# Performance work log

Measured on AMD Instinct MI355X. Metric: run time of the kernel, lower is better.

Reference implementation:

```python
import jax, jax.numpy as jnp
import numpy as np

N = 100000      # nodes
E = 1600000     # message-passing edges
P = 1000000     # prediction edges
DIN = 128       # node_in_channels
H = 128         # hidden_channels
DOUT = 64       # out_channels (node embedding)
EIN = 32        # edge_in_channels
EPS = 1e-5


def setup_inputs() -> dict:
    key = jax.random.key(0)
    ks = iter(jax.random.split(key, 48))
    nk = lambda: next(ks)
    rn = lambda shape: jax.random.normal(nk(), shape, dtype=jnp.float32)
    glorot = lambda shape: rn(shape) * (1.0 / np.sqrt(shape[-1]))
    inp = {
        "x": rn((N, DIN)),
        "edge_index": jax.random.randint(nk(), (2, E), 0, N),
        "pred_edge_index": jax.random.randint(nk(), (2, P), 0, N),
        "edge_features": rn((P, EIN)),
        # SAGEConv layer 1: lin_l (aggregated, with bias), lin_r (root, no bias)
        "sage1_Wl": glorot((H, DIN)), "sage1_bl": jnp.zeros((H,), jnp.float32), "sage1_Wr": glorot((H, DIN)),
        "bn1_g": jnp.ones((H,), jnp.float32), "bn1_b": jnp.zeros((H,), jnp.float32),
        "bn1_m": rn((H,)) * 0.1, "bn1_v": jnp.ones((H,), jnp.float32),
        # SAGEConv layer 2
        "sage2_Wl": glorot((DOUT, H)), "sage2_bl": jnp.zeros((DOUT,), jnp.float32), "sage2_Wr": glorot((DOUT, H)),
        # edge MLP: Linear(EIN, H//2) -> BN -> ReLU -> Linear(H//2, H//4)
        "edge_W1": glorot((H // 2, EIN)), "edge_b1": jnp.zeros((H // 2,), jnp.float32),
        "ebn_g": jnp.ones((H // 2,), jnp.float32), "ebn_b": jnp.zeros((H // 2,), jnp.float32),
        "ebn_m": rn((H // 2,)) * 0.1, "ebn_v": jnp.ones((H // 2,), jnp.float32),
        "edge_W2": glorot((H // 4, H // 2)), "edge_b2": jnp.zeros((H // 4,), jnp.float32),
        # predictor: Linear(2*DOUT+H//4, H) -> BN -> ReLU -> Linear(H, H//2) -> BN -> ReLU -> Linear(H//2, 1)
        "p_W1": glorot((H, 2 * DOUT + H // 4)), "p_b1": jnp.zeros((H,), jnp.float32),
        "pbn1_g": jnp.ones((H,), jnp.float32), "pbn1_b": jnp.zeros((H,), jnp.float32),
        "pbn1_m": rn((H,)) * 0.1, "pbn1_v": jnp.ones((H,), jnp.float32),
        "p_W2": glorot((H // 2, H)), "p_b2": jnp.zeros((H // 2,), jnp.float32),
        "pbn2_g": jnp.ones((H // 2,), jnp.float32), "pbn2_b": jnp.zeros((H // 2,), jnp.float32),
        "pbn2_m": rn((H // 2,)) * 0.1, "pbn2_v": jnp.ones((H // 2,), jnp.float32),
        "p_W3": glorot((1, H // 2)), "p_b3": jnp.zeros((1,), jnp.float32),
    }
    return inp


def _bn(h, g, b, m, v):
    # eval-mode BatchNorm1d with running stats
    return (h - m) * (g / jnp.sqrt(v + EPS)) + b


def _sage(h, src, dst, Wl, bl, Wr):
    # PyG SAGEConv (mean aggr): lin_l(mean of h[src] at dst) + lin_r(h)
    msg = jax.ops.segment_sum(h[src], dst, num_segments=N)        # [N, d]
    cnt = jax.ops.segment_sum(jnp.ones((src.shape[0],), h.dtype), dst, num_segments=N)
    agg = msg / jnp.maximum(cnt, 1.0)[:, None]
    return agg @ Wl.T + bl + h @ Wr.T


def reference(x, edge_index, pred_edge_index, edge_features,
              sage1_Wl, sage1_bl, sage1_Wr, bn1_g, bn1_b, bn1_m, bn1_v,
              sage2_Wl, sage2_bl, sage2_Wr,
              edge_W1, edge_b1, ebn_g, ebn_b, ebn_m, ebn_v, edge_W2, edge_b2,
              p_W1, p_b1, pbn1_g, pbn1_b, pbn1_m, pbn1_v,
              p_W2, p_b2, pbn2_g, pbn2_b, pbn2_m, pbn2_v, p_W3, p_b3):
    src, dst = edge_index[0], edge_index[1]
    # GraphSAGE encoder (eval mode: dropout off, BN running stats)
    h = _sage(x, src, dst, sage1_Wl, sage1_bl, sage1_Wr)
    h = jax.nn.relu(_bn(h, bn1_g, bn1_b, bn1_m, bn1_v))
    z = _sage(h, src, dst, sage2_Wl, sage2_bl, sage2_Wr)          # [N, DOUT]
    # edge-pair gather + concat
    combined = jnp.concatenate([z[pred_edge_index[0]], z[pred_edge_index[1]]], axis=-1)  # [P, 2*DOUT]
    # edge feature MLP
    e = edge_features @ edge_W1.T + edge_b1
    e = jax.nn.relu(_bn(e, ebn_g, ebn_b, ebn_m, ebn_v))
    e = e @ edge_W2.T + edge_b2                                   # [P, H//4]
    combined = jnp.concatenate([combined, e], axis=-1)            # [P, 2*DOUT + H//4]
    # predictor MLP
    u = combined @ p_W1.T + p_b1
    u = jax.nn.relu(_bn(u, pbn1_g, pbn1_b, pbn1_m, pbn1_v))
    u = u @ p_W2.T + p_b2
    u = jax.nn.relu(_bn(u, pbn2_g, pbn2_b, pbn2_m, pbn2_v))
    out = u @ p_W3.T + p_b3                                       # [P, 1]
    return out[:, 0]
```

## Files before the change

### kernel.cpp

```cpp
#include <hip/hip_runtime.h>

#define Nn 100000
#define Ee 1600000
#define Pp 1000000
#define EPSf 1e-5f

typedef _Float16 f16x8 __attribute__((ext_vector_type(8)));
typedef _Float16 f16x4 __attribute__((ext_vector_type(4)));
typedef _Float16 f16x2 __attribute__((ext_vector_type(2)));
typedef float f32x4 __attribute__((ext_vector_type(4)));

__device__ __forceinline__ float4 ld4(const float* p) { return *(const float4*)p; }

#define oW1l 0
#define oW1r 16384
#define oW2l 32768
#define oW2r 40960
#define oW1a 49152
#define oW1b 57344
#define oW1c 65536
#define oWe1 69632
#define oWe2 71680
#define oWp2 73728
#define W16_TOTAL 81920

#define BN_TOTAL 608

#define BSH 9
#define NB2 196
#define SCAP2 9216
#define ECHUNK 4096
#define NCHUNK ((Ee + ECHUNK - 1) / ECHUNK)

__global__ __launch_bounds__(256) void prep_kernel(
    const float* __restrict__ x,
    const float* __restrict__ s1Wl, const float* __restrict__ s1Wr,
    const float* __restrict__ s2Wl, const float* __restrict__ s2Wr,
    const float* __restrict__ pW1,  const float* __restrict__ eW1,
    const float* __restrict__ eW2,  const float* __restrict__ pW2,
    const float* __restrict__ eb1,
    const float* __restrict__ ebng, const float* __restrict__ ebnb,
    const float* __restrict__ ebnm, const float* __restrict__ ebnv,
    const float* __restrict__ eb2,
    const float* __restrict__ pb1,
    const float* __restrict__ p1g, const float* __restrict__ p1b,
    const float* __restrict__ p1m, const float* __restrict__ p1v,
    const float* __restrict__ pb2,
    const float* __restrict__ p2g, const float* __restrict__ p2b,
    const float* __restrict__ p2m, const float* __restrict__ p2v,
    const float* __restrict__ pW3,
    _Float16* __restrict__ w16, float* __restrict__ bnA,
    _Float16* __restrict__ x16) {
    int tid = blockIdx.x * 256 + threadIdx.x;
    if (tid < W16_TOTAL) {
        float v;
        if (tid < 16384)      v = s1Wl[tid];
        else if (tid < 32768) v = s1Wr[tid - 16384];
        else if (tid < 40960) v = s2Wl[tid - 32768];
        else if (tid < 49152) v = s2Wr[tid - 40960];
        else if (tid < 57344) { int l = tid - 49152; v = pW1[(l >> 6) * 160 + (l & 63)]; }
        else if (tid < 65536) { int l = tid - 57344; v = pW1[(l >> 6) * 160 + 64 + (l & 63)]; }
        else if (tid < 69632) { int l = tid - 65536; v = pW1[(l >> 5) * 160 + 128 + (l & 31)]; }
        else if (tid < 71680) v = eW1[tid - 69632];
        else if (tid < 73728) v = eW2[tid - 71680];
        else                  v = pW2[tid - 73728];
        w16[tid] = (_Float16)v;
    } else if (tid < W16_TOTAL + BN_TOTAL) {
        int b = tid - W16_TOTAL;
        float v;
        if (b < 64)       v = ebng[b] * rsqrtf(ebnv[b] + EPSf);
        else if (b < 128) { int c = b - 64;  float s = ebng[c] * rsqrtf(ebnv[c] + EPSf);
                            v = (eb1[c] - ebnm[c]) * s + ebnb[c]; }
        else if (b < 256) { int c = b - 128; v = p1g[c] * rsqrtf(p1v[c] + EPSf); }
        else if (b < 384) { int c = b - 256; float s = p1g[c] * rsqrtf(p1v[c] + EPSf);
                            v = (pb1[c] - p1m[c]) * s + p1b[c]; }
        else if (b < 448) { int c = b - 384; v = p2g[c] * rsqrtf(p2v[c] + EPSf); }
        else if (b < 512) { int c = b - 448; float s = p2g[c] * rsqrtf(p2v[c] + EPSf);
                            v = (pb2[c] - p2m[c]) * s + p2b[c]; }
        else if (b < 544) v = eb2[b - 512];
        else              v = pW3[b - 544];
        bnA[b] = v;
    }
    int stride = gridDim.x * 256;
    const int NV = Nn * 128 / 4;
    for (int i = tid; i < NV; i += stride) {
        float4 v = ((const float4*)x)[i];
        f16x4 h = {(_Float16)v.x, (_Float16)v.y, (_Float16)v.z, (_Float16)v.w};
        ((f16x4*)x16)[i] = h;
    }
}

__global__ __launch_bounds__(256) void bucketA_kernel(
    const int* __restrict__ src, const int* __restrict__ dst,
    unsigned* __restrict__ stage, unsigned* __restrict__ gcur) {
    __shared__ unsigned hist[NB2];
    __shared__ unsigned base[NB2];
    const int t = threadIdx.x;
    const int e0 = blockIdx.x * ECHUNK;
    for (int u = t; u < NB2; u += 256) hist[u] = 0u;
    __syncthreads();

    int sv[16], dv[16];
#pragma unroll
    for (int k = 0; k < 16; ++k) {
        int e = e0 + k * 256 + t;
        if (e < Ee) {
            sv[k] = src[e];
            dv[k] = dst[e];
            atomicAdd(&hist[dv[k] >> BSH], 1u);
        } else dv[k] = -1;
    }
    __syncthreads();
    for (int u = t; u < NB2; u += 256) {
        unsigned h = hist[u];
        base[u] = h ? atomicAdd(&gcur[u], h) : 0u;
        hist[u] = 0u;
    }
    __syncthreads();
#pragma unroll
    for (int k = 0; k < 16; ++k) {
        if (dv[k] >= 0) {
            int b = dv[k] >> BSH;
            unsigned p = atomicAdd(&hist[b], 1u);
            stage[(size_t)b * SCAP2 + base[b] + p] =
                ((unsigned)sv[k] << BSH) | (unsigned)(dv[k] & 511);
        }
    }
}

__global__ __launch_bounds__(256) void countC_kernel(
    const unsigned* __restrict__ stage, const unsigned* __restrict__ gcur,
    unsigned* __restrict__ deg) {
    __shared__ unsigned cnt[512];
    const int b = blockIdx.x;
    const int t = threadIdx.x;
    cnt[t] = 0u; cnt[t + 256] = 0u;
    __syncthreads();
    unsigned m = gcur[b];
    const unsigned* sp = stage + (size_t)b * SCAP2;
    for (unsigned i = t; i < m; i += 256)
        atomicAdd(&cnt[sp[i] & 511], 1u);
    __syncthreads();
    int n0 = b << BSH;
    if (n0 + t < Nn)       deg[n0 + t] = cnt[t];
    if (n0 + 256 + t < Nn) deg[n0 + 256 + t] = cnt[t + 256];
}

__global__ __launch_bounds__(1024) void scanA_kernel(const unsigned* __restrict__ deg,
                                                     unsigned* __restrict__ escan,
                                                     unsigned* __restrict__ bsum) {
    __shared__ unsigned s[1024];
    int t = threadIdx.x;
    int gid = blockIdx.x * 1024 + t;
    unsigned v = (gid < Nn) ? deg[gid] : 0u;
    s[t] = v;
    __syncthreads();
    for (int off = 1; off < 1024; off <<= 1) {
        unsigned u = (t >= off) ? s[t - off] : 0u;
        __syncthreads();
        s[t] += u;
        __syncthreads();
    }
    if (gid < Nn) escan[gid] = s[t] - v;
    if (t == 1023) bsum[blockIdx.x] = s[1023];
}

__global__ __launch_bounds__(128) void scanB_kernel(const unsigned* __restrict__ bsum,
                                                    unsigned* __restrict__ boff,
                                                    int nblk) {
    __shared__ unsigned s[128];
    int t = threadIdx.x;
    unsigned v = (t < nblk) ? bsum[t] : 0u;
    s[t] = v;
    __syncthreads();
    for (int off = 1; off < 128; off <<= 1) {
        unsigned u = (t >= off) ? s[t - off] : 0u;
        __syncthreads();
        s[t] += u;
        __syncthreads();
    }
    if (t < nblk) boff[t] = s[t] - v;
}

__global__ __launch_bounds__(1024) void scanC_kernel(const unsigned* __restrict__ escan,
                                                     const unsigned* __restrict__ boff,
                                                     int* __restrict__ rowptr) {
    int t = threadIdx.x;
    int gid = blockIdx.x * 1024 + t;
    if (gid < Nn) rowptr[gid] = (int)(escan[gid] + boff[blockIdx.x]);
    if (gid == 0) rowptr[Nn] = Ee;
}

__global__ __launch_bounds__(256) void scatterE_kernel(
    const unsigned* __restrict__ stage, const unsigned* __restrict__ gcur,
    const int* __restrict__ rowptr, int* __restrict__ elist) {
    __shared__ int lbase[512];
    __shared__ unsigned cur[512];
    const int b = blockIdx.x;
    const int t = threadIdx.x;
    const int n0 = b << BSH;
    lbase[t]       = (n0 + t < Nn)       ? rowptr[n0 + t]       : 0;
    lbase[t + 256] = (n0 + 256 + t < Nn) ? rowptr[n0 + 256 + t] : 0;
    cur[t] = 0u; cur[t + 256] = 0u;
    __syncthreads();
    unsigned m = gcur[b];
    const unsigned* sp = stage + (size_t)b * SCAP2;
    for (unsigned i = t; i < m; i += 256) {
        unsigned v = sp[i];
        int lid = v & 511;
        unsigned p = atomicAdd(&cur[lid], 1u);
        elist[lbase[lid] + p] = (int)(v >> BSH);
    }
}

template<int W>
__global__ __launch_bounds__(256, 8) void aggregate16_kernel(
    const _Float16* __restrict__ feat,
    const int* __restrict__ rowptr,
    const int* __restrict__ elist,
    _Float16* __restrict__ outp) {
    int node = (blockIdx.x * 256 + threadIdx.x) >> 6;
    int lane = threadIdx.x & 63;
    if (node >= Nn) return;
    constexpr int SEGS = W / 8;
    constexpr int RPI  = 64 / SEGS;
    const int r = lane / SEGS, c = lane % SEGS;
    int beg = rowptr[node], end = rowptr[node + 1];
    int n = end - beg;
    float acc[8];
#pragma unroll
    for (int k = 0; k < 8; ++k) acc[k] = 0.f;
    for (int c0 = 0; c0 < n; c0 += 64) {
        int m = min(64, n - c0);
        int se = (lane < m) ? elist[beg + c0 + lane] : 0;
        int iters = (m + RPI - 1) / RPI;
#pragma unroll 4
        for (int i = 0; i < iters; ++i) {
            int j = i * RPI + r;
            int s = __shfl(se, j);
            if (j < m) {
                f16x8 v = *(const f16x8*)(feat + (size_t)s * W + c * 8);
#pragma unroll
                for (int k = 0; k < 8; ++k) acc[k] += (float)v[k];
            }
        }
    }
#pragma unroll
    for (int k = 0; k < 8; ++k) {
#pragma unroll
        for (int off = SEGS; off < 64; off <<= 1)
            acc[k] += __shfl_xor(acc[k], off);
    }
    if (r == 0) {
        float inv = 1.0f / fmaxf((float)n, 1.0f);
        f16x8 o;
#pragma unroll
        for (int k = 0; k < 8; ++k) o[k] = (_Float16)(acc[k] * inv);
        *(f16x8*)(outp + (size_t)node * W + c * 8) = o;
    }
}

__global__ __launch_bounds__(256) void dense1_kernel(
    const _Float16* __restrict__ A1, const _Float16* __restrict__ A2,
    const _Float16* __restrict__ W1, const _Float16* __restrict__ W2,
    const float* __restrict__ lb,
    const float* __restrict__ bng, const float* __restrict__ bnb,
    const float* __restrict__ bnm, const float* __restrict__ bnv,
    _Float16* __restrict__ out) {
    const int t = threadIdx.x;
    const int w = t >> 6, lane = t & 63;
    const int lrow = lane & 15, lq = lane >> 4;
    const int row0 = blockIdx.x * 64 + w * 16;
    const int ld = min(row0 + lrow, Nn - 1);

    f16x8 a1[4], a2[4];
#pragma unroll
    for (int i = 0; i < 4; ++i) {
        a1[i] = *(const f16x8*)(A1 + (size_t)ld * 128 + i * 32 + lq * 8);
        a2[i] = *(const f16x8*)(A2 + (size_t)ld * 128 + i * 32 + lq * 8);
    }
#pragma unroll
    for (int nt = 0; nt < 8; ++nt) {
        const _Float16* w1r = W1 + (size_t)(nt * 16 + lrow) * 128;
        const _Float16* w2r = W2 + (size_t)(nt * 16 + lrow) * 128;
        f32x4 c = {0.f, 0.f, 0.f, 0.f};
#pragma unroll
        for (int i = 0; i < 4; ++i) {
            c = __builtin_amdgcn_mfma_f32_16x16x32_f16(a1[i], *(const f16x8*)(w1r + i * 32 + lq * 8), c, 0, 0, 0);
            c = __builtin_amdgcn_mfma_f32_16x16x32_f16(a2[i], *(const f16x8*)(w2r + i * 32 + lq * 8), c, 0, 0, 0);
        }
        int cc = nt * 16 + lrow;
        float s = bng[cc] * rsqrtf(bnv[cc] + EPSf);
        float h = (lb[cc] - bnm[cc]) * s + bnb[cc];
#pragma unroll
        for (int r = 0; r < 4; ++r) {
            int gr = row0 + lq * 4 + r;
            if (gr < Nn)
                out[(size_t)gr * 128 + cc] = (_Float16)fmaxf(c[r] * s + h, 0.f);
        }
    }
}

__global__ __launch_bounds__(256) void gemmY_kernel(
    const _Float16* __restrict__ A, const _Float16* __restrict__ W,
    _Float16* __restrict__ out) {
    const int t = threadIdx.x;
    const int w = t >> 6, lane = t & 63;
    const int lrow = lane & 15, lq = lane >> 4;
    const int row0 = blockIdx.x * 64 + w * 16;
    const int ld = min(row0 + lrow, Nn - 1);
    f16x8 a[4];
#pragma unroll
    for (int i = 0; i < 4; ++i)
        a[i] = *(const f16x8*)(A + (size_t)ld * 128 + i * 32 + lq * 8);
#pragma unroll
    for (int nt = 0; nt < 4; ++nt) {
        const _Float16* wr = W + (size_t)(nt * 16 + lrow) * 128;
        f32x4 c = {0.f, 0.f, 0.f, 0.f};
#pragma unroll
        for (int i = 0; i < 4; ++i)
            c = __builtin_amdgcn_mfma_f32_16x16x32_f16(a[i], *(const f16x8*)(wr + i * 32 + lq * 8), c, 0, 0, 0);
        int cc = nt * 16 + lrow;
#pragma unroll
        for (int r = 0; r < 4; ++r) {
            int gr = row0 + lq * 4 + r;
            if (gr < Nn) out[(size_t)gr * 64 + cc] = (_Float16)c[r];
        }
    }
}

__global__ __launch_bounds__(256) void dense2b_kernel(
    const _Float16* __restrict__ aggY, const _Float16* __restrict__ A2,
    const _Float16* __restrict__ W2, const float* __restrict__ lb,
    _Float16* __restrict__ out) {
    const int t = threadIdx.x;
    const int w = t >> 6, lane = t & 63;
    const int lrow = lane & 15, lq = lane >> 4;
    const int row0 = blockIdx.x * 64 + w * 16;
    const int ld = min(row0 + lrow, Nn - 1);
    f16x8 a[4];
#pragma unroll
    for (int i = 0; i < 4; ++i)
        a[i] = *(const f16x8*)(A2 + (size_t)ld * 128 + i * 32 + lq * 8);
#pragma unroll
    for (int nt = 0; nt < 4; ++nt) {
        const _Float16* wr = W2 + (size_t)(nt * 16 + lrow) * 128;
        f32x4 c = {0.f, 0.f, 0.f, 0.f};
#pragma unroll
        for (int i = 0; i < 4; ++i)
            c = __builtin_amdgcn_mfma_f32_16x16x32_f16(a[i], *(const f16x8*)(wr + i * 32 + lq * 8), c, 0, 0, 0);
        int cc = nt * 16 + lrow;
        float b = lb[cc];
#pragma unroll
        for (int r = 0; r < 4; ++r) {
            int gr = row0 + lq * 4 + r;
            if (gr < Nn) {
                float g = (float)aggY[(size_t)gr * 64 + cc];
                out[(size_t)gr * 64 + cc] = (_Float16)(c[r] + g + b);
            }
        }
    }
}

__global__ __launch_bounds__(256) void emlp_kernel(
    const float* __restrict__ ef,
    const _Float16* __restrict__ w16,
    const float* __restrict__ bnA,
    _Float16* __restrict__ e2out) {
    __shared__ __align__(16) _Float16 E1[64 * 72];
    const int t = threadIdx.x;
    const int lane = t & 63, w = t >> 6;
    const int lrow = lane & 15, lq = lane >> 4;
    const int e0 = blockIdx.x * 64 + w * 16;
    const int erow = w * 16 + lrow;

    const float* src = ef + (size_t)(e0 + lrow) * 32 + lq * 8;
    float4 f0 = ld4(src), f1 = ld4(src + 4);
    f16x8 bf = {(_Float16)f0.x, (_Float16)f0.y, (_Float16)f0.z, (_Float16)f0.w,
                (_Float16)f1.x, (_Float16)f1.y, (_Float16)f1.z, (_Float16)f1.w};

#pragma unroll
    for (int nt = 0; nt < 4; ++nt) {
        f16x8 wf = *(const f16x8*)(w16 + oWe1 + (nt * 16 + lrow) * 32 + lq * 8);
        f32x4 c = {0.f, 0.f, 0.f, 0.f};
        c = __builtin_amdgcn_mfma_f32_16x16x32_f16(wf, bf, c, 0, 0, 0);
        int cb = nt * 16 + lq * 4;
        float4 s = *(const float4*)(bnA + cb);
        float4 h = *(const float4*)(bnA + 64 + cb);
        f16x4 o;
        o[0] = (_Float16)fmaxf(c[0] * s.x + h.x, 0.f);
        o[1] = (_Float16)fmaxf(c[1] * s.y + h.y, 0.f);
        o[2] = (_Float16)fmaxf(c[2] * s.z + h.z, 0.f);
        o[3] = (_Float16)fmaxf(c[3] * s.w + h.w, 0.f);
        *(f16x4*)(E1 + erow * 72 + cb) = o;
    }
    f16x8 a0 = *(const f16x8*)(E1 + erow * 72 + lq * 8);
    f16x8 a1 = *(const f16x8*)(E1 + erow * 72 + 32 + lq * 8);
#pragma unroll
    for (int nt = 0; nt < 2; ++nt) {
        f16x8 b0 = *(const f16x8*)(w16 + oWe2 + (nt * 16 + lrow) * 64 + lq * 8);
        f16x8 b1 = *(const f16x8*)(w16 + oWe2 + (nt * 16 + lrow) * 64 + 32 + lq * 8);
        f32x4 c = {0.f, 0.f, 0.f, 0.f};
        c = __builtin_amdgcn_mfma_f32_16x16x32_f16(b0, a0, c, 0, 0, 0);
        c = __builtin_amdgcn_mfma_f32_16x16x32_f16(b1, a1, c, 0, 0, 0);
        int cb = nt * 16 + lq * 4;
        float4 bias = *(const float4*)(bnA + 512 + cb);
        f16x4 o;
        o[0] = (_Float16)(c[0] + bias.x);
        o[1] = (_Float16)(c[1] + bias.y);
        o[2] = (_Float16)(c[2] + bias.z);
        o[3] = (_Float16)(c[3] + bias.w);
        *(f16x4*)(e2out + (size_t)(e0 + lrow) * 32 + cb) = o;
    }
}

#define EPB 256
#define NT  ((Pp + EPB - 1) / EPB)
#define EGRID 256

#define oL_W1a 0
#define oL_W1b 18432
#define oL_W1c 36864
#define oL_Wp2 47104
#define oL_BN  64512
#define oL_ZU  66304
#define SMEM_BYTES 135936

__global__ __launch_bounds__(1024, 4) void edge_kernel(
    const int* __restrict__ pe,
    const _Float16* __restrict__ e2,
    const _Float16* __restrict__ z,
    const _Float16* __restrict__ w16,
    const float* __restrict__ bnA,
    const float* __restrict__ pb3,
    float* __restrict__ out) {
    __shared__ __align__(16) unsigned char smem[SMEM_BYTES];
    _Float16* LW1a = (_Float16*)(smem + oL_W1a);
    _Float16* LW1b = (_Float16*)(smem + oL_W1b);
    _Float16* LW1c = (_Float16*)(smem + oL_W1c);
    _Float16* LWp2 = (_Float16*)(smem + oL_Wp2);
    float*    LBN  = (float*)(smem + oL_BN);
    _Float16* ZU   = (_Float16*)(smem + oL_ZU);

    const float* bn2s = LBN;        const float* bn2h = LBN + 128;
    const float* bn3s = LBN + 256;  const float* bn3h = LBN + 320;
    const float* wp3g = LBN + 384;

    const int t = threadIdx.x;
    const int lane = t & 63;
    const int w = t >> 6;
    const int m0 = w * 16;
    const int lrow = lane & 15;
    const int lq = lane >> 4;
    const float pb3v = pb3[0];

    auto load_idx = [&](int tl, int& ia, int& ib) {
        int e = min(tl * EPB + m0 + lrow, Pp - 1);
        ia = pe[e];
        ib = pe[Pp + e];
    };
    auto gather = [&](int tl, int ia, int ib, f16x8* F) {
        F[0] = *(const f16x8*)(z + (size_t)ia * 64 + lq * 8);
        F[1] = *(const f16x8*)(z + (size_t)ia * 64 + 32 + lq * 8);
        F[2] = *(const f16x8*)(z + (size_t)ib * 64 + lq * 8);
        F[3] = *(const f16x8*)(z + (size_t)ib * 64 + 32 + lq * 8);
        int e = min(tl * EPB + m0 + lrow, Pp - 1);
        F[4] = *(const f16x8*)(e2 + (size_t)e * 32 + lq * 8);
    };

    int tile = blockIdx.x;
    int ia1, ib1;
    {
        int ia0, ib0;
        load_idx(tile, ia0, ib0);
        load_idx(tile + EGRID, ia1, ib1);
        f16x8 F[5];
        gather(tile, ia0, ib0, F);

        { int r = t >> 3, s = t & 7;
          *(f16x8*)(LW1a + r * 72 + s * 8) = *(const f16x8*)(w16 + oW1a + r * 64 + s * 8);
          *(f16x8*)(LW1b + r * 72 + s * 8) = *(const f16x8*)(w16 + oW1b + r * 64 + s * 8); }
        if (t < 512) { int r = t >> 2, s = t & 3;
          *(f16x8*)(LW1c + r * 40 + s * 8) = *(const f16x8*)(w16 + oW1c + r * 32 + s * 8); }
        { int r = t >> 4, s = t & 15;
          *(f16x8*)(LWp2 + r * 136 + s * 8) = *(const f16x8*)(w16 + oWp2 + r * 128 + s * 8); }
        if (t < 384) LBN[t] = bnA[128 + t];
        else if (t < 448) LBN[t] = bnA[544 + (t - 384)];
        __syncthreads();

        const int erow = m0 + lrow;
        const int zr = erow * 136;
        for (; tile < NT; tile += EGRID) {
            f16x8 G[5];
            gather(tile + EGRID, ia1, ib1, G);
            int ia2, ib2;
            load_idx(tile + 2 * EGRID, ia2, ib2);

            const bool act = (tile * EPB + m0) < Pp;
            if (act) {
                __builtin_amdgcn_s_setprio(1);
#pragma unroll
                for (int nt = 0; nt < 8; ++nt) {
                    const _Float16* wa = LW1a + (nt * 16 + lrow) * 72;
                    const _Float16* wb = LW1b + (nt * 16 + lrow) * 72;
                    const _Float16* wc = LW1c + (nt * 16 + lrow) * 40;
                    f32x4 c = {0.f, 0.f, 0.f, 0.f};
                    c = __builtin_amdgcn_mfma_f32_16x16x32_f16(*(const f16x8*)(wa + lq * 8),      F[0], c, 0, 0, 0);
                    c = __builtin_amdgcn_mfma_f32_16x16x32_f16(*(const f16x8*)(wa + 32 + lq * 8), F[1], c, 0, 0, 0);
                    c = __builtin_amdgcn_mfma_f32_16x16x32_f16(*(const f16x8*)(wb + lq * 8),      F[2], c, 0, 0, 0);
                    c = __builtin_amdgcn_mfma_f32_16x16x32_f16(*(const f16x8*)(wb + 32 + lq * 8), F[3], c, 0, 0, 0);
                    c = __builtin_amdgcn_mfma_f32_16x16x32_f16(*(const f16x8*)(wc + lq * 8),      F[4], c, 0, 0, 0);
                    int cb = nt * 16 + lq * 4;
                    float4 s = *(const float4*)(bn2s + cb);
                    float4 h = *(const float4*)(bn2h + cb);
                    f16x4 o;
                    o[0] = (_Float16)fmaxf(c[0] * s.x + h.x, 0.f);
                    o[1] = (_Float16)fmaxf(c[1] * s.y + h.y, 0.f);
                    o[2] = (_Float16)fmaxf(c[2] * s.z + h.z, 0.f);
                    o[3] = (_Float16)fmaxf(c[3] * s.w + h.w, 0.f);
                    *(f16x4*)(ZU + zr + cb) = o;
                }
                __builtin_amdgcn_s_setprio(0);
                {
                    f16x8 a0 = *(const f16x8*)(ZU + zr + 0  + lq * 8);
                    f16x8 a1 = *(const f16x8*)(ZU + zr + 32 + lq * 8);
                    f16x8 a2 = *(const f16x8*)(ZU + zr + 64 + lq * 8);
                    f16x8 a3 = *(const f16x8*)(ZU + zr + 96 + lq * 8);
                    float acc = 0.f;
                    __builtin_amdgcn_s_setprio(1);
#pragma unroll
                    for (int nt = 0; nt < 4; ++nt) {
                        const _Float16* wr = LWp2 + (nt * 16 + lrow) * 136 + lq * 8;
                        f32x4 c = {0.f, 0.f, 0.f, 0.f};
                        c = __builtin_amdgcn_mfma_f32_16x16x32_f16(*(const f16x8*)(wr + 0),  a0, c, 0, 0, 0);
                        c = __builtin_amdgcn_mfma_f32_16x16x32_f16(*(const f16x8*)(wr + 32), a1, c, 0, 0, 0);
                        c = __builtin_amdgcn_mfma_f32_16x16x32_f16(*(const f16x8*)(wr + 64), a2, c, 0, 0, 0);
                        c = __builtin_amdgcn_mfma_f32_16x16x32_f16(*(const f16x8*)(wr + 96), a3, c, 0, 0, 0);
                        int cb = nt * 16 + lq * 4;
                        float4 s  = *(const float4*)(bn3s + cb);
                        float4 h  = *(const float4*)(bn3h + cb);
                        float4 w3 = *(const float4*)(wp3g + cb);
                        acc += fmaxf(c[0] * s.x + h.x, 0.f) * w3.x;
                        acc += fmaxf(c[1] * s.y + h.y, 0.f) * w3.y;
                        acc += fmaxf(c[2] * s.z + h.z, 0.f) * w3.z;
                        acc += fmaxf(c[3] * s.w + h.w, 0.f) * w3.w;
                    }
                    __builtin_amdgcn_s_setprio(0);
                    acc += __shfl_xor(acc, 16);
                    acc += __shfl_xor(acc, 32);
                    if (lane < 16) out[tile * EPB + m0 + lane] = acc + pb3v;
                }
            }
#pragma unroll
            for (int i = 0; i < 5; ++i) F[i] = G[i];
            ia1 = ia2; ib1 = ib2;
        }
    }
}

extern "C" void kernel_launch(void* const* d_in, const int* in_sizes, int n_in,
                              void* d_out, int out_size, void* d_ws, size_t ws_size,
                              hipStream_t stream) {
    const float* x    = (const float*)d_in[0];
    const int*   eidx = (const int*)d_in[1];
    const int*   pe   = (const int*)d_in[2];
    const float* ef   = (const float*)d_in[3];
    const float* s1Wl = (const float*)d_in[4];
    const float* s1bl = (const float*)d_in[5];
    const float* s1Wr = (const float*)d_in[6];
    const float* bn1g = (const float*)d_in[7];
    const float* bn1b = (const float*)d_in[8];
    const float* bn1m = (const float*)d_in[9];
    const float* bn1v = (const float*)d_in[10];
    const float* s2Wl = (const float*)d_in[11];
    const float* s2bl = (const float*)d_in[12];
    const float* s2Wr = (const float*)d_in[13];
    const float* eW1  = (const float*)d_in[14];
    const float* eb1  = (const float*)d_in[15];
    const float* ebng = (const float*)d_in[16];
    const float* ebnb = (const float*)d_in[17];
    const float* ebnm = (const float*)d_in[18];
    const float* ebnv = (const float*)d_in[19];
    const float* eW2  = (const float*)d_in[20];
    const float* eb2  = (const float*)d_in[21];
    const float* pW1  = (const float*)d_in[22];
    const float* pb1  = (const float*)d_in[23];
    const float* p1g  = (const float*)d_in[24];
    const float* p1b  = (const float*)d_in[25];
    const float* p1m  = (const float*)d_in[26];
    const float* p1v  = (const float*)d_in[27];
    const float* pW2  = (const float*)d_in[28];
    const float* pb2  = (const float*)d_in[29];
    const float* p2g  = (const float*)d_in[30];
    const float* p2b  = (const float*)d_in[31];
    const float* p2m  = (const float*)d_in[32];
    const float* p2v  = (const float*)d_in[33];
    const float* pW3  = (const float*)d_in[34];
    const float* pb3  = (const float*)d_in[35];
    float* out = (float*)d_out;

    char* wk = (char*)d_ws;
    auto carve = [&](size_t bytes) {
        char* p = wk;
        wk += (bytes + 255) & ~(size_t)255;
        return p;
    };
    unsigned*  deg    = (unsigned*)carve((size_t)Nn * 4);
    unsigned*  gcur   = (unsigned*)carve((size_t)256 * 4);
    int*       rowptr = (int*)carve((size_t)(Nn + 1) * 4);
    int*       elist  = (int*)carve((size_t)Ee * 4);
    unsigned*  escan  = (unsigned*)carve((size_t)Nn * 4);
    unsigned*  bsum   = (unsigned*)carve(128 * 4);
    unsigned*  boff   = (unsigned*)carve(128 * 4);
    _Float16*  w16    = (_Float16*)carve((size_t)W16_TOTAL * 2);
    float*     bnA    = (float*)carve((size_t)BN_TOTAL * 4);
    _Float16*  bufX   = (_Float16*)carve((size_t)Nn * 128 * 2);
    _Float16*  bufA   = (_Float16*)carve((size_t)Nn * 128 * 2);
    _Float16*  bufH   = (_Float16*)carve((size_t)Nn * 128 * 2);
    _Float16*  e2buf  = (_Float16*)carve((size_t)Pp * 32 * 2);
    _Float16*  bufY   = bufX;
    _Float16*  bufZ   = bufX + (size_t)Nn * 64;
    _Float16*  bufAy  = bufA;
    unsigned*  stage  = (unsigned*)bufH;

    const int* e_src = eidx;
    const int* e_dst = eidx + Ee;
    const int SBLK = (Nn + 1023) / 1024;

    hipMemsetAsync(gcur, 0, 256 * 4, stream);

    prep_kernel<<<800, 256, 0, stream>>>(x, s1Wl, s1Wr, s2Wl, s2Wr, pW1, eW1, eW2, pW2,
                                         eb1, ebng, ebnb, ebnm, ebnv, eb2,
                                         pb1, p1g, p1b, p1m, p1v,
                                         pb2, p2g, p2b, p2m, p2v, pW3,
                                         w16, bnA, bufX);
    emlp_kernel<<<Pp / 64, 256, 0, stream>>>(ef, w16, bnA, e2buf);

    bucketA_kernel<<<NCHUNK, 256, 0, stream>>>(e_src, e_dst, stage, gcur);
    countC_kernel<<<NB2, 256, 0, stream>>>(stage, gcur, deg);
    scanA_kernel<<<SBLK, 1024, 0, stream>>>(deg, escan, bsum);
    scanB_kernel<<<1, 128, 0, stream>>>(bsum, boff, SBLK);
    scanC_kernel<<<SBLK, 1024, 0, stream>>>(escan, boff, rowptr);
    scatterE_kernel<<<NB2, 256, 0, stream>>>(stage, gcur, rowptr, elist);

    aggregate16_kernel<128><<<Nn / 4, 256, 0, stream>>>(bufX, rowptr, elist, bufA);
    dense1_kernel<<<(Nn + 63) / 64, 256, 0, stream>>>(
        bufA, bufX, w16 + oW1l, w16 + oW1r, s1bl, bn1g, bn1b, bn1m, bn1v, bufH);

    gemmY_kernel<<<(Nn + 63) / 64, 256, 0, stream>>>(bufH, w16 + oW2l, bufY);
    aggregate16_kernel<64><<<Nn / 4, 256, 0, stream>>>(bufY, rowptr, elist, bufAy);
    dense2b_kernel<<<(Nn + 63) / 64, 256, 0, stream>>>(
        bufAy, bufH, w16 + oW2r, s2bl, bufZ);

    edge_kernel<<<EGRID, 1024, 0, stream>>>(pe, e2buf, bufZ, w16, bnA, pb3, out);
}
```

Before: 670.6 us.

## Merge preprocessing kernels, collapse CSR scans, and fuse dense1 with layer-2 GEMM

Prep, edge-feature MLP and edge bucketing now run as one heterogeneous launch, with blocks dispatched by index range. The emlp branch reads fp32 weights and BN parameters directly instead of waiting for prep output. The count, three-stage scan and scatter sequence becomes a single 196-entry bucket scan plus a scatter kernel that builds local prefix sums and writes rowptr itself. dense1 keeps the hidden tile in shared memory and computes the layer-2 Y projection in the same kernel, which removes the gemmY launch and a full re-read of H. Output stores are vectorised by swapping MFMA operand order. The cost is more register and shared-memory pressure in the merged kernels and redundant weight conversion in every emlp block.

```diff
diff --git a/kernel.cpp b/kernel.cpp
--- a/kernel.cpp
+++ b/kernel.cpp
@@ -7,7 +7,6 @@
 
 typedef _Float16 f16x8 __attribute__((ext_vector_type(8)));
 typedef _Float16 f16x4 __attribute__((ext_vector_type(4)));
-typedef _Float16 f16x2 __attribute__((ext_vector_type(2)));
 typedef float f32x4 __attribute__((ext_vector_type(4)));
 
 __device__ __forceinline__ float4 ld4(const float* p) { return *(const float4*)p; }
@@ -32,7 +31,11 @@
 #define ECHUNK 4096
 #define NCHUNK ((Ee + ECHUNK - 1) / ECHUNK)
 
-__global__ __launch_bounds__(256) void prep_kernel(
+#define EMLP_B (Pp / 64)
+#define PREP_B 800
+#define PH1_GRID (NCHUNK + EMLP_B + PREP_B)
+
+__global__ __launch_bounds__(256) void phase1_kernel(
     const float* __restrict__ x,
     const float* __restrict__ s1Wl, const float* __restrict__ s1Wr,
     const float* __restrict__ s2Wl, const float* __restrict__ s2Wr,
@@ -50,161 +53,193 @@
     const float* __restrict__ p2m, const float* __restrict__ p2v,
     const float* __restrict__ pW3,
     _Float16* __restrict__ w16, float* __restrict__ bnA,
-    _Float16* __restrict__ x16) {
-    int tid = blockIdx.x * 256 + threadIdx.x;
-    if (tid < W16_TOTAL) {
-        float v;
-        if (tid < 16384)      v = s1Wl[tid];
-        else if (tid < 32768) v = s1Wr[tid - 16384];
-        else if (tid < 40960) v = s2Wl[tid - 32768];
-        else if (tid < 49152) v = s2Wr[tid - 40960];
-        else if (tid < 57344) { int l = tid - 49152; v = pW1[(l >> 6) * 160 + (l & 63)]; }
-        else if (tid < 65536) { int l = tid - 57344; v = pW1[(l >> 6) * 160 + 64 + (l & 63)]; }
-        else if (tid < 69632) { int l = tid - 65536; v = pW1[(l >> 5) * 160 + 128 + (l & 31)]; }
-        else if (tid < 71680) v = eW1[tid - 69632];
-        else if (tid < 73728) v = eW2[tid - 71680];
-        else                  v = pW2[tid - 73728];
-        w16[tid] = (_Float16)v;
-    } else if (tid < W16_TOTAL + BN_TOTAL) {
-        int b = tid - W16_TOTAL;
-        float v;
-        if (b < 64)       v = ebng[b] * rsqrtf(ebnv[b] + EPSf);
-        else if (b < 128) { int c = b - 64;  float s = ebng[c] * rsqrtf(ebnv[c] + EPSf);
-                            v = (eb1[c] - ebnm[c]) * s + ebnb[c]; }
-        else if (b < 256) { int c = b - 128; v = p1g[c] * rsqrtf(p1v[c] + EPSf); }
-        else if (b < 384) { int c = b - 256; float s = p1g[c] * rsqrtf(p1v[c] + EPSf);
-                            v = (pb1[c] - p1m[c]) * s + p1b[c]; }
-        else if (b < 448) { int c = b - 384; v = p2g[c] * rsqrtf(p2v[c] + EPSf); }
-        else if (b < 512) { int c = b - 448; float s = p2g[c] * rsqrtf(p2v[c] + EPSf);
-                            v = (pb2[c] - p2m[c]) * s + p2b[c]; }
-        else if (b < 544) v = eb2[b - 512];
-        else              v = pW3[b - 544];
-        bnA[b] = v;
-    }
-    int stride = gridDim.x * 256;
-    const int NV = Nn * 128 / 4;
-    for (int i = tid; i < NV; i += stride) {
-        float4 v = ((const float4*)x)[i];
-        f16x4 h = {(_Float16)v.x, (_Float16)v.y, (_Float16)v.z, (_Float16)v.w};
-        ((f16x4*)x16)[i] = h;
-    }
-}
-
-__global__ __launch_bounds__(256) void bucketA_kernel(
-    const int* __restrict__ src, const int* __restrict__ dst,
-    unsigned* __restrict__ stage, unsigned* __restrict__ gcur) {
-    __shared__ unsigned hist[NB2];
-    __shared__ unsigned base[NB2];
+    _Float16* __restrict__ x16,
+    const int* __restrict__ esrc, const int* __restrict__ edst,
+    unsigned* __restrict__ stage, unsigned* __restrict__ gcur,
+    const float* __restrict__ ef, _Float16* __restrict__ e2out) {
+    __shared__ __align__(16) unsigned char sm[9216];
+    const int bb = blockIdx.x;
     const int t = threadIdx.x;
-    const int e0 = blockIdx.x * ECHUNK;
-    for (int u = t; u < NB2; u += 256) hist[u] = 0u;
+
+    if (bb < NCHUNK) {
+        unsigned* hist = (unsigned*)sm;
+        unsigned* base = hist + NB2;
+        const int e0 = bb * ECHUNK;
+        for (int u = t; u < NB2; u += 256) hist[u] = 0u;
+        __syncthreads();
+        int sv[16], dv[16];
+#pragma unroll
+        for (int k = 0; k < 16; ++k) {
+            int e = e0 + k * 256 + t;
+            if (e < Ee) {
+                sv[k] = esrc[e];
+                dv[k] = edst[e];
+                atomicAdd(&hist[dv[k] >> BSH], 1u);
+            } else dv[k] = -1;
+        }
+        __syncthreads();
+        for (int u = t; u < NB2; u += 256) {
+            unsigned h = hist[u];
+            base[u] = h ? atomicAdd(&gcur[u], h) : 0u;
+            hist[u] = 0u;
+        }
+        __syncthreads();
+#pragma unroll
+        for (int k = 0; k < 16; ++k) {
+            if (dv[k] >= 0) {
+                int b = dv[k] >> BSH;
+                unsigned p = atomicAdd(&hist[b], 1u);
+                stage[(size_t)b * SCAP2 + base[b] + p] =
+                    ((unsigned)sv[k] << BSH) | (unsigned)(dv[k] & 511);
+            }
+        }
+    } else if (bb < NCHUNK + EMLP_B) {
+        _Float16* E1 = (_Float16*)sm;
+        const int lane = t & 63, w = t >> 6;
+        const int lrow = lane & 15, lq = lane >> 4;
+        const int e0 = (bb - NCHUNK) * 64 + w * 16;
+        const int erow = w * 16 + lrow;
+
+        const float* src = ef + (size_t)(e0 + lrow) * 32 + lq * 8;
+        float4 f0 = ld4(src), f1 = ld4(src + 4);
+        f16x8 bf = {(_Float16)f0.x, (_Float16)f0.y, (_Float16)f0.z, (_Float16)f0.w,
+                    (_Float16)f1.x, (_Float16)f1.y, (_Float16)f1.z, (_Float16)f1.w};
+#pragma unroll
+        for (int nt = 0; nt < 4; ++nt) {
+            const float* wp = eW1 + (nt * 16 + lrow) * 32 + lq * 8;
+            float4 w0 = ld4(wp), w1 = ld4(wp + 4);
+            f16x8 wf = {(_Float16)w0.x, (_Float16)w0.y, (_Float16)w0.z, (_Float16)w0.w,
+                        (_Float16)w1.x, (_Float16)w1.y, (_Float16)w1.z, (_Float16)w1.w};
+            f32x4 c = {0.f, 0.f, 0.f, 0.f};
+            c = __builtin_amdgcn_mfma_f32_16x16x32_f16(wf, bf, c, 0, 0, 0);
+            int cb = nt * 16 + lq * 4;
+            float4 g = ld4(ebng + cb), vv = ld4(ebnv + cb);
+            float4 b_ = ld4(ebnb + cb), mm = ld4(ebnm + cb), b1 = ld4(eb1 + cb);
+            float sx = g.x * rsqrtf(vv.x + EPSf), hx = (b1.x - mm.x) * sx + b_.x;
+            float sy = g.y * rsqrtf(vv.y + EPSf), hy = (b1.y - mm.y) * sy + b_.y;
+            float sz = g.z * rsqrtf(vv.z + EPSf), hz = (b1.z - mm.z) * sz + b_.z;
+            float sw = g.w * rsqrtf(vv.w + EPSf), hw = (b1.w - mm.w) * sw + b_.w;
+            f16x4 o;
+            o[0] = (_Float16)fmaxf(c[0] * sx + hx, 0.f);
+            o[1] = (_Float16)fmaxf(c[1] * sy + hy, 0.f);
+            o[2] = (_Float16)fmaxf(c[2] * sz + hz, 0.f);
+            o[3] = (_Float16)fmaxf(c[3] * sw + hw, 0.f);
+            *(f16x4*)(E1 + erow * 72 + cb) = o;
+        }
+        f16x8 a0 = *(const f16x8*)(E1 + erow * 72 + lq * 8);
+        f16x8 a1 = *(const f16x8*)(E1 + erow * 72 + 32 + lq * 8);
+#pragma unroll
+        for (int nt = 0; nt < 2; ++nt) {
+            const float* wp = eW2 + (nt * 16 + lrow) * 64 + lq * 8;
+            float4 p0 = ld4(wp), p1 = ld4(wp + 4);
+            float4 q0 = ld4(wp + 32), q1 = ld4(wp + 36);
+            f16x8 b0 = {(_Float16)p0.x, (_Float16)p0.y, (_Float16)p0.z, (_Float16)p0.w,
+                        (_Float16)p1.x, (_Float16)p1.y, (_Float16)p1.z, (_Float16)p1.w};
+            f16x8 b1 = {(_Float16)q0.x, (_Float16)q0.y, (_Float16)q0.z, (_Float16)q0.w,
+                        (_Float16)q1.x, (_Float16)q1.y, (_Float16)q1.z, (_Float16)q1.w};
+            f32x4 c = {0.f, 0.f, 0.f, 0.f};
+            c = __builtin_amdgcn_mfma_f32_16x16x32_f16(b0, a0, c, 0, 0, 0);
+            c = __builtin_amdgcn_mfma_f32_16x16x32_f16(b1, a1, c, 0, 0, 0);
+            int cb = nt * 16 + lq * 4;
+            float4 bias = ld4(eb2 + cb);
+            f16x4 o;
+            o[0] = (_Float16)(c[0] + bias.x);
+            o[1] = (_Float16)(c[1] + bias.y);
+            o[2] = (_Float16)(c[2] + bias.z);
+            o[3] = (_Float16)(c[3] + bias.w);
+            *(f16x4*)(e2out + (size_t)(e0 + lrow) * 32 + cb) = o;
+        }
+    } else {
+        int tid = (bb - NCHUNK - EMLP_B) * 256 + t;
+        if (tid < W16_TOTAL) {
+            float v;
+            if (tid < 16384)      v = s1Wl[tid];
+            else if (tid < 32768) v = s1Wr[tid - 16384];
+            else if (tid < 40960) v = s2Wl[tid - 32768];
+            else if (tid < 49152) v = s2Wr[tid - 40960];
+            else if (tid < 57344) { int l = tid - 49152; v = pW1[(l >> 6) * 160 + (l & 63)]; }
+            else if (tid < 65536) { int l = tid - 57344; v = pW1[(l >> 6) * 160 + 64 + (l & 63)]; }
+            else if (tid < 69632) { int l = tid - 65536; v = pW1[(l >> 5) * 160 + 128 + (l & 31)]; }
+            else if (tid < 71680) v = eW1[tid - 69632];
+            else if (tid < 73728) v = eW2[tid - 71680];
+            else                  v = pW2[tid - 73728];
+            w16[tid] = (_Float16)v;
+        } else if (tid < W16_TOTAL + BN_TOTAL) {
+            int b = tid - W16_TOTAL;
+            float v;
+            if (b < 64)       v = ebng[b] * rsqrtf(ebnv[b] + EPSf);
+            else if (b < 128) { int c = b - 64;  float s = ebng[c] * rsqrtf(ebnv[c] + EPSf);
+                                v = (eb1[c] - ebnm[c]) * s + ebnb[c]; }
+            else if (b < 256) { int c = b - 128; v = p1g[c] * rsqrtf(p1v[c] + EPSf); }
+            else if (b < 384) { int c = b - 256; float s = p1g[c] * rsqrtf(p1v[c] + EPSf);
+                                v = (pb1[c] - p1m[c]) * s + p1b[c]; }
+            else if (b < 448) { int c = b - 384; v = p2g[c] * rsqrtf(p2v[c] + EPSf); }
+            else if (b < 512) { int c = b - 448; float s = p2g[c] * rsqrtf(p2v[c] + EPSf);
+                                v = (pb2[c] - p2m[c]) * s + p2b[c]; }
+            else if (b < 544) v = eb2[b - 512];
+            else              v = pW3[b - 544];
+            bnA[b] = v;
+        }
+        const int NV = Nn * 128 / 4;
+        for (int i = tid; i < NV; i += PREP_B * 256) {
+            float4 v = ((const float4*)x)[i];
+            f16x4 h = {(_Float16)v.x, (_Float16)v.y, (_Float16)v.z, (_Float16)v.w};
+            ((f16x4*)x16)[i] = h;
+        }
+    }
+}
+
+__global__ __launch_bounds__(256) void scanG_kernel(const unsigned* __restrict__ gcur,
+                                                    unsigned* __restrict__ gbase,
+                                                    int* __restrict__ rowptr) {
+    __shared__ unsigned s[256];
+    int t = threadIdx.x;
+    unsigned v = (t < NB2) ? gcur[t] : 0u;
+    s[t] = v;
     __syncthreads();
-
-    int sv[16], dv[16];
-#pragma unroll
-    for (int k = 0; k < 16; ++k) {
-        int e = e0 + k * 256 + t;
-        if (e < Ee) {
-            sv[k] = src[e];
-            dv[k] = dst[e];
-            atomicAdd(&hist[dv[k] >> BSH], 1u);
-        } else dv[k] = -1;
-    }
-    __syncthreads();
-    for (int u = t; u < NB2; u += 256) {
-        unsigned h = hist[u];
-        base[u] = h ? atomicAdd(&gcur[u], h) : 0u;
-        hist[u] = 0u;
-    }
-    __syncthreads();
-#pragma unroll
-    for (int k = 0; k < 16; ++k) {
-        if (dv[k] >= 0) {
-            int b = dv[k] >> BSH;
-            unsigned p = atomicAdd(&hist[b], 1u);
-            stage[(size_t)b * SCAP2 + base[b] + p] =
-                ((unsigned)sv[k] << BSH) | (unsigned)(dv[k] & 511);
-        }
-    }
-}
-
-__global__ __launch_bounds__(256) void countC_kernel(
+    for (int off = 1; off < 256; off <<= 1) {
+        unsigned u = (t >= off) ? s[t - off] : 0u;
+        __syncthreads();
+        s[t] += u;
+        __syncthreads();
+    }
+    if (t < NB2) gbase[t] = s[t] - v;
+    if (t == 0) rowptr[Nn] = Ee;
+}
+
+__global__ __launch_bounds__(256) void scatterE2_kernel(
     const unsigned* __restrict__ stage, const unsigned* __restrict__ gcur,
-    unsigned* __restrict__ deg) {
+    const unsigned* __restrict__ gbase,
+    int* __restrict__ rowptr, int* __restrict__ elist) {
     __shared__ unsigned cnt[512];
+    __shared__ unsigned cur[512];
+    __shared__ int lbase[512];
     const int b = blockIdx.x;
     const int t = threadIdx.x;
+    const int n0 = b << BSH;
     cnt[t] = 0u; cnt[t + 256] = 0u;
     __syncthreads();
-    unsigned m = gcur[b];
+    const unsigned m = gcur[b];
     const unsigned* sp = stage + (size_t)b * SCAP2;
     for (unsigned i = t; i < m; i += 256)
         atomicAdd(&cnt[sp[i] & 511], 1u);
     __syncthreads();
-    int n0 = b << BSH;
-    if (n0 + t < Nn)       deg[n0 + t] = cnt[t];
-    if (n0 + 256 + t < Nn) deg[n0 + 256 + t] = cnt[t + 256];
-}
-
-__global__ __launch_bounds__(1024) void scanA_kernel(const unsigned* __restrict__ deg,
-                                                     unsigned* __restrict__ escan,
-                                                     unsigned* __restrict__ bsum) {
-    __shared__ unsigned s[1024];
-    int t = threadIdx.x;
-    int gid = blockIdx.x * 1024 + t;
-    unsigned v = (gid < Nn) ? deg[gid] : 0u;
-    s[t] = v;
+    unsigned o0 = cnt[t], o1 = cnt[t + 256];
+    for (int off = 1; off < 512; off <<= 1) {
+        unsigned a0 = (t >= off) ? cnt[t - off] : 0u;
+        unsigned a1 = ((t + 256) >= off) ? cnt[t + 256 - off] : 0u;
+        __syncthreads();
+        cnt[t] += a0; cnt[t + 256] += a1;
+        __syncthreads();
+    }
+    const unsigned gb = gbase[b];
+    int r0 = (int)(gb + cnt[t] - o0);
+    int r1 = (int)(gb + cnt[t + 256] - o1);
+    lbase[t] = r0; lbase[t + 256] = r1;
+    cur[t] = 0u; cur[t + 256] = 0u;
+    if (n0 + t < Nn)       rowptr[n0 + t] = r0;
+    if (n0 + 256 + t < Nn) rowptr[n0 + 256 + t] = r1;
     __syncthreads();
-    for (int off = 1; off < 1024; off <<= 1) {
-        unsigned u = (t >= off) ? s[t - off] : 0u;
-        __syncthreads();
-        s[t] += u;
-        __syncthreads();
-    }
-    if (gid < Nn) escan[gid] = s[t] - v;
-    if (t == 1023) bsum[blockIdx.x] = s[1023];
-}
-
-__global__ __launch_bounds__(128) void scanB_kernel(const unsigned* __restrict__ bsum,
-                                                    unsigned* __restrict__ boff,
-                                                    int nblk) {
-    __shared__ unsigned s[128];
-    int t = threadIdx.x;
-    unsigned v = (t < nblk) ? bsum[t] : 0u;
-    s[t] = v;
-    __syncthreads();
-    for (int off = 1; off < 128; off <<= 1) {
-        unsigned u = (t >= off) ? s[t - off] : 0u;
-        __syncthreads();
-        s[t] += u;
-        __syncthreads();
-    }
-    if (t < nblk) boff[t] = s[t] - v;
-}
-
-__global__ __launch_bounds__(1024) void scanC_kernel(const unsigned* __restrict__ escan,
-                                                     const unsigned* __restrict__ boff,
-                                                     int* __restrict__ rowptr) {
-    int t = threadIdx.x;
-    int gid = blockIdx.x * 1024 + t;
-    if (gid < Nn) rowptr[gid] = (int)(escan[gid] + boff[blockIdx.x]);
-    if (gid == 0) rowptr[Nn] = Ee;
-}
-
-__global__ __launch_bounds__(256) void scatterE_kernel(
-    const unsigned* __restrict__ stage, const unsigned* __restrict__ gcur,
-    const int* __restrict__ rowptr, int* __restrict__ elist) {
-    __shared__ int lbase[512];
-    __shared__ unsigned cur[512];
-    const int b = blockIdx.x;
-    const int t = threadIdx.x;
-    const int n0 = b << BSH;
-    lbase[t]       = (n0 + t < Nn)       ? rowptr[n0 + t]       : 0;
-    lbase[t + 256] = (n0 + 256 + t < Nn) ? rowptr[n0 + 256 + t] : 0;
-    cur[t] = 0u; cur[t + 256] = 0u;
-    __syncthreads();
-    unsigned m = gcur[b];
-    const unsigned* sp = stage + (size_t)b * SCAP2;
     for (unsigned i = t; i < m; i += 256) {
         unsigned v = sp[i];
         int lid = v & 511;
@@ -260,18 +295,21 @@
     }
 }
 
-__global__ __launch_bounds__(256) void dense1_kernel(
+__global__ __launch_bounds__(256) void dense1g_kernel(
     const _Float16* __restrict__ A1, const _Float16* __restrict__ A2,
     const _Float16* __restrict__ W1, const _Float16* __restrict__ W2,
+    const _Float16* __restrict__ Wy,
     const float* __restrict__ lb,
     const float* __restrict__ bng, const float* __restrict__ bnb,
     const float* __restrict__ bnm, const float* __restrict__ bnv,
-    _Float16* __restrict__ out) {
+    _Float16* __restrict__ outh, _Float16* __restrict__ outy) {
+    __shared__ __align__(16) _Float16 HL[64 * 136];
     const int t = threadIdx.x;
     const int w = t >> 6, lane = t & 63;
     const int lrow = lane & 15, lq = lane >> 4;
     const int row0 = blockIdx.x * 64 + w * 16;
     const int ld = min(row0 + lrow, Nn - 1);
+    const bool rowok = (row0 + lrow) < Nn;
 
     f16x8 a1[4], a2[4];
 #pragma unroll
@@ -286,46 +324,41 @@
         f32x4 c = {0.f, 0.f, 0.f, 0.f};
 #pragma unroll
         for (int i = 0; i < 4; ++i) {
-            c = __builtin_amdgcn_mfma_f32_16x16x32_f16(a1[i], *(const f16x8*)(w1r + i * 32 + lq * 8), c, 0, 0, 0);
-            c = __builtin_amdgcn_mfma_f32_16x16x32_f16(a2[i], *(const f16x8*)(w2r + i * 32 + lq * 8), c, 0, 0, 0);
-        }
-        int cc = nt * 16 + lrow;
-        float s = bng[cc] * rsqrtf(bnv[cc] + EPSf);
-        float h = (lb[cc] - bnm[cc]) * s + bnb[cc];
-#pragma unroll
-        for (int r = 0; r < 4; ++r) {
-            int gr = row0 + lq * 4 + r;
-            if (gr < Nn)
-                out[(size_t)gr * 128 + cc] = (_Float16)fmaxf(c[r] * s + h, 0.f);
-        }
-    }
-}
-
-__global__ __launch_bounds__(256) void gemmY_kernel(
-    const _Float16* __restrict__ A, const _Float16* __restrict__ W,
-    _Float16* __restrict__ out) {
-    const int t = threadIdx.x;
-    const int w = t >> 6, lane = t & 63;
-    const int lrow = lane & 15, lq = lane >> 4;
-    const int row0 = blockIdx.x * 64 + w * 16;
-    const int ld = min(row0 + lrow, Nn - 1);
+            c = __builtin_amdgcn_mfma_f32_16x16x32_f16(*(const f16x8*)(w1r + i * 32 + lq * 8), a1[i], c, 0, 0, 0);
+            c = __builtin_amdgcn_mfma_f32_16x16x32_f16(*(const f16x8*)(w2r + i * 32 + lq * 8), a2[i], c, 0, 0, 0);
+        }
+        int cb = nt * 16 + lq * 4;
+        float4 g = ld4(bng + cb), vv = ld4(bnv + cb);
+        float4 bb = ld4(bnb + cb), mm = ld4(bnm + cb), lv = ld4(lb + cb);
+        float sx = g.x * rsqrtf(vv.x + EPSf), hx = (lv.x - mm.x) * sx + bb.x;
+        float sy = g.y * rsqrtf(vv.y + EPSf), hy = (lv.y - mm.y) * sy + bb.y;
+        float sz = g.z * rsqrtf(vv.z + EPSf), hz = (lv.z - mm.z) * sz + bb.z;
+        float sw = g.w * rsqrtf(vv.w + EPSf), hw = (lv.w - mm.w) * sw + bb.w;
+        f16x4 o;
+        o[0] = (_Float16)fmaxf(c[0] * sx + hx, 0.f);
+        o[1] = (_Float16)fmaxf(c[1] * sy + hy, 0.f);
+        o[2] = (_Float16)fmaxf(c[2] * sz + hz, 0.f);
+        o[3] = (_Float16)fmaxf(c[3] * sw + hw, 0.f);
+        *(f16x4*)(HL + (w * 16 + lrow) * 136 + cb) = o;
+        if (rowok) *(f16x4*)(outh + (size_t)(row0 + lrow) * 128 + cb) = o;
+    }
+    __syncthreads();
     f16x8 a[4];
 #pragma unroll
     for (int i = 0; i < 4; ++i)
-        a[i] = *(const f16x8*)(A + (size_t)ld * 128 + i * 32 + lq * 8);
+        a[i] = *(const f16x8*)(HL + (w * 16 + lrow) * 136 + i * 32 + lq * 8);
 #pragma unroll
     for (int nt = 0; nt < 4; ++nt) {
-        const _Float16* wr = W + (size_t)(nt * 16 + lrow) * 128;
+        const _Float16* wr = Wy + (size_t)(nt * 16 + lrow) * 128;
         f32x4 c = {0.f, 0.f, 0.f, 0.f};
 #pragma unroll
         for (int i = 0; i < 4; ++i)
-            c = __builtin_amdgcn_mfma_f32_16x16x32_f16(a[i], *(const f16x8*)(wr + i * 32 + lq * 8), c, 0, 0, 0);
-        int cc = nt * 16 + lrow;
-#pragma unroll
-        for (int r = 0; r < 4; ++r) {
-            int gr = row0 + lq * 4 + r;
-            if (gr < Nn) out[(size_t)gr * 64 + cc] = (_Float16)c[r];
-        }
+            c = __builtin_amdgcn_mfma_f32_16x16x32_f16(*(const f16x8*)(wr + i * 32 + lq * 8), a[i], c, 0, 0, 0);
+        int cb = nt * 16 + lq * 4;
+        f16x4 o;
+        o[0] = (_Float16)c[0]; o[1] = (_Float16)c[1];
+        o[2] = (_Float16)c[2]; o[3] = (_Float16)c[3];
+        if (rowok) *(f16x4*)(outy + (size_t)(row0 + lrow) * 64 + cb) = o;
     }
 }
 
@@ -338,6 +371,7 @@
     const int lrow = lane & 15, lq = lane >> 4;
     const int row0 = blockIdx.x * 64 + w * 16;
     const int ld = min(row0 + lrow, Nn - 1);
+    const bool rowok = (row0 + lrow) < Nn;
     f16x8 a[4];
 #pragma unroll
     for (int i = 0; i < 4; ++i)
@@ -348,69 +382,16 @@
         f32x4 c = {0.f, 0.f, 0.f, 0.f};
 #pragma unroll
         for (int i = 0; i < 4; ++i)
-            c = __builtin_amdgcn_mfma_f32_16x16x32_f16(a[i], *(const f16x8*)(wr + i * 32 + lq * 8), c, 0, 0, 0);
-        int cc = nt * 16 + lrow;
-        float b = lb[cc];
-#pragma unroll
-        for (int r = 0; r < 4; ++r) {
-            int gr = row0 + lq * 4 + r;
-            if (gr < Nn) {
-                float g = (float)aggY[(size_t)gr * 64 + cc];
-                out[(size_t)gr * 64 + cc] = (_Float16)(c[r] + g + b);
-            }
-        }
-    }
-}
-
-__global__ __launch_bounds__(256) void emlp_kernel(
-    const float* __restrict__ ef,
-    const _Float16* __restrict__ w16,
-    const float* __restrict__ bnA,
-    _Float16* __restrict__ e2out) {
-    __shared__ __align__(16) _Float16 E1[64 * 72];
-    const int t = threadIdx.x;
-    const int lane = t & 63, w = t >> 6;
-    const int lrow = lane & 15, lq = lane >> 4;
-    const int e0 = blockIdx.x * 64 + w * 16;
-    const int erow = w * 16 + lrow;
-
-    const float* src = ef + (size_t)(e0 + lrow) * 32 + lq * 8;
-    float4 f0 = ld4(src), f1 = ld4(src + 4);
-    f16x8 bf = {(_Float16)f0.x, (_Float16)f0.y, (_Float16)f0.z, (_Float16)f0.w,
-                (_Float16)f1.x, (_Float16)f1.y, (_Float16)f1.z, (_Float16)f1.w};
-
-#pragma unroll
-    for (int nt = 0; nt < 4; ++nt) {
-        f16x8 wf = *(const f16x8*)(w16 + oWe1 + (nt * 16 + lrow) * 32 + lq * 8);
-        f32x4 c = {0.f, 0.f, 0.f, 0.f};
-        c = __builtin_amdgcn_mfma_f32_16x16x32_f16(wf, bf, c, 0, 0, 0);
+            c = __builtin_amdgcn_mfma_f32_16x16x32_f16(*(const f16x8*)(wr + i * 32 + lq * 8), a[i], c, 0, 0, 0);
         int cb = nt * 16 + lq * 4;
-        float4 s = *(const float4*)(bnA + cb);
-        float4 h = *(const float4*)(bnA + 64 + cb);
+        float4 bv = ld4(lb + cb);
+        f16x4 g4 = *(const f16x4*)(aggY + (size_t)ld * 64 + cb);
         f16x4 o;
-        o[0] = (_Float16)fmaxf(c[0] * s.x + h.x, 0.f);
-        o[1] = (_Float16)fmaxf(c[1] * s.y + h.y, 0.f);
-        o[2] = (_Float16)fmaxf(c[2] * s.z + h.z, 0.f);
-        o[3] = (_Float16)fmaxf(c[3] * s.w + h.w, 0.f);
-        *(f16x4*)(E1 + erow * 72 + cb) = o;
-    }
-    f16x8 a0 = *(const f16x8*)(E1 + erow * 72 + lq * 8);
-    f16x8 a1 = *(const f16x8*)(E1 + erow * 72 + 32 + lq * 8);
-#pragma unroll
-    for (int nt = 0; nt < 2; ++nt) {
-        f16x8 b0 = *(const f16x8*)(w16 + oWe2 + (nt * 16 + lrow) * 64 + lq * 8);
-        f16x8 b1 = *(const f16x8*)(w16 + oWe2 + (nt * 16 + lrow) * 64 + 32 + lq * 8);
-        f32x4 c = {0.f, 0.f, 0.f, 0.f};
-        c = __builtin_amdgcn_mfma_f32_16x16x32_f16(b0, a0, c, 0, 0, 0);
-        c = __builtin_amdgcn_mfma_f32_16x16x32_f16(b1, a1, c, 0, 0, 0);
-        int cb = nt * 16 + lq * 4;
-        float4 bias = *(const float4*)(bnA + 512 + cb);
-        f16x4 o;
-        o[0] = (_Float16)(c[0] + bias.x);
-        o[1] = (_Float16)(c[1] + bias.y);
-        o[2] = (_Float16)(c[2] + bias.z);
-        o[3] = (_Float16)(c[3] + bias.w);
-        *(f16x4*)(e2out + (size_t)(e0 + lrow) * 32 + cb) = o;
+        o[0] = (_Float16)(c[0] + (float)g4[0] + bv.x);
+        o[1] = (_Float16)(c[1] + (float)g4[1] + bv.y);
+        o[2] = (_Float16)(c[2] + (float)g4[2] + bv.z);
+        o[3] = (_Float16)(c[3] + (float)g4[3] + bv.w);
+        if (rowok) *(f16x4*)(out + (size_t)(row0 + lrow) * 64 + cb) = o;
     }
 }
 
@@ -605,13 +586,10 @@
         wk += (bytes + 255) & ~(size_t)255;
         return p;
     };
-    unsigned*  deg    = (unsigned*)carve((size_t)Nn * 4);
     unsigned*  gcur   = (unsigned*)carve((size_t)256 * 4);
+    unsigned*  gbase  = (unsigned*)carve((size_t)256 * 4);
     int*       rowptr = (int*)carve((size_t)(Nn + 1) * 4);
     int*       elist  = (int*)carve((size_t)Ee * 4);
-    unsigned*  escan  = (unsigned*)carve((size_t)Nn * 4);
-    unsigned*  bsum   = (unsigned*)carve(128 * 4);
-    unsigned*  boff   = (unsigned*)carve(128 * 4);
     _Float16*  w16    = (_Float16*)carve((size_t)W16_TOTAL * 2);
     float*     bnA    = (float*)carve((size_t)BN_TOTAL * 4);
     _Float16*  bufX   = (_Float16*)carve((size_t)Nn * 128 * 2);
@@ -625,29 +603,26 @@
 
     const int* e_src = eidx;
     const int* e_dst = eidx + Ee;
-    const int SBLK = (Nn + 1023) / 1024;
 
     hipMemsetAsync(gcur, 0, 256 * 4, stream);
 
-    prep_kernel<<<800, 256, 0, stream>>>(x, s1Wl, s1Wr, s2Wl, s2Wr, pW1, eW1, eW2, pW2,
-                                         eb1, ebng, ebnb, ebnm, ebnv, eb2,
-                                         pb1, p1g, p1b, p1m, p1v,
-                                         pb2, p2g, p2b, p2m, p2v, pW3,
-                                         w16, bnA, bufX);
-    emlp_kernel<<<Pp / 64, 256, 0, stream>>>(ef, w16, bnA, e2buf);
-
-    bucketA_kernel<<<NCHUNK, 256, 0, stream>>>(e_src, e_dst, stage, gcur);
-    countC_kernel<<<NB2, 256, 0, stream>>>(stage, gcur, deg);
-    scanA_kernel<<<SBLK, 1024, 0, stream>>>(deg, escan, bsum);
-    scanB_kernel<<<1, 128, 0, stream>>>(bsum, boff, SBLK);
-    scanC_kernel<<<SBLK, 1024, 0, stream>>>(escan, boff, rowptr);
-    scatterE_kernel<<<NB2, 256, 0, stream>>>(stage, gcur, rowptr, elist);
+    phase1_kernel<<<PH1_GRID, 256, 0, stream>>>(
+        x, s1Wl, s1Wr, s2Wl, s2Wr, pW1, eW1, eW2, pW2,
+        eb1, ebng, ebnb, ebnm, ebnv, eb2,
+        pb1, p1g, p1b, p1m, p1v,
+        pb2, p2g, p2b, p2m, p2v, pW3,
+        w16, bnA, bufX,
+        e_src, e_dst, stage, gcur,
+        ef, e2buf);
+
+    scanG_kernel<<<1, 256, 0, stream>>>(gcur, gbase, rowptr);
+    scatterE2_kernel<<<NB2, 256, 0, stream>>>(stage, gcur, gbase, rowptr, elist);
 
     aggregate16_kernel<128><<<Nn / 4, 256, 0, stream>>>(bufX, rowptr, elist, bufA);
-    dense1_kernel<<<(Nn + 63) / 64, 256, 0, stream>>>(
-        bufA, bufX, w16 + oW1l, w16 + oW1r, s1bl, bn1g, bn1b, bn1m, bn1v, bufH);
-
-    gemmY_kernel<<<(Nn + 63) / 64, 256, 0, stream>>>(bufH, w16 + oW2l, bufY);
+    dense1g_kernel<<<(Nn + 63) / 64, 256, 0, stream>>>(
+        bufA, bufX, w16 + oW1l, w16 + oW1r, w16 + oW2l,
+        s1bl, bn1g, bn1b, bn1m, bn1v, bufH, bufY);
+
     aggregate16_kernel<64><<<Nn / 4, 256, 0, stream>>>(bufY, rowptr, elist, bufAy);
     dense2b_kernel<<<(Nn + 63) / 64, 256, 0, stream>>>(
         bufAy, bufH, w16 + oW2r, s2bl, bufZ);
```

Result: slower. 729.2 us (+8.7%).
